# Optimization experiments

Hardware: AMD Instinct MI355X
Metric: run time of the kernel (lower is better)

Reference implementation:

```python
import jax, jax.numpy as jnp
import numpy as np
import math

INPUT_SIZE = 1024
HIDDEN_SIZE = 1024
RANK = 256
BATCH = 32
SEQ = 512


def setup_inputs() -> dict:
    key = jax.random.key(0)
    k_x, k_a, k_b, k_c = jax.random.split(key, 4)
    stdv = 1.0 / math.sqrt(HIDDEN_SIZE)
    x = jax.random.normal(k_x, (BATCH, SEQ, INPUT_SIZE), dtype=jnp.float32)
    a = jax.random.uniform(k_a, (HIDDEN_SIZE, RANK * 4), minval=-stdv, maxval=stdv, dtype=jnp.float32)
    b = jax.random.uniform(k_b, (INPUT_SIZE, RANK * 4), minval=-stdv, maxval=stdv, dtype=jnp.float32)
    ct = jax.random.uniform(k_c, (RANK * 4, HIDDEN_SIZE), minval=-stdv, maxval=stdv, dtype=jnp.float32)
    return {"x": x, "a": a, "b": b, "ct": ct}


def reference(x, a, b, ct):
    B, S, _ = x.shape
    H = a.shape[0]
    R = a.shape[1] // 4
    ct3 = ct.reshape(4, R, H)  # (4, R, H)
    # Precompute input projection for all timesteps: (B, S, 4R)
    xb = jnp.einsum('bsi,ir->bsr', x, b)

    def step(carry, xb_t):
        h, c = carry
        g = (h @ a) * xb_t                      # (B, 4R)
        g = jnp.einsum('bkr,krh->bkh', g.reshape(B, 4, R), ct3)  # (B, 4, H)
        f_t = jax.nn.sigmoid(g[:, 0])
        i_t = jax.nn.sigmoid(g[:, 1])
        g_t = jnp.tanh(g[:, 2])
        o_t = jax.nn.sigmoid(g[:, 3])
        c = f_t * c + i_t * g_t
        h = o_t * jnp.tanh(c)
        return (h, c), h

    h0 = jnp.zeros((B, H), dtype=x.dtype)
    c0 = jnp.zeros((B, H), dtype=x.dtype)
    (h_t, c_t), hs = jax.lax.scan(step, (h0, c0), jnp.swapaxes(xb, 0, 1))
    hidden_seq = jnp.swapaxes(hs, 0, 1)  # (B, S, H)
    return hidden_seq, (h_t, c_t)
```

## Files before the change

kernel.cpp:

```cpp
#include <hip/hip_runtime.h>
#include <math.h>

#define NTHR 512
typedef unsigned long long u64;

__device__ __forceinline__ void st_uc(float* p, float v) {
    asm volatile("global_store_dword %0, %1, off sc0 sc1" :: "v"(p), "v"(v) : "memory");
}
#define LGKM0_BAR do { \
    asm volatile("s_waitcnt lgkmcnt(0)" ::: "memory"); \
    __builtin_amdgcn_s_barrier(); \
} while (0)

__global__ void init_kernel(u64* hp, u64* gp) {
    int i = blockIdx.x * blockDim.x + threadIdx.x;
    if (i < 65536) {
        __hip_atomic_store(hp + i, 0xFFFFFFFF00000000ull, __ATOMIC_RELAXED, __HIP_MEMORY_SCOPE_AGENT);
        __hip_atomic_store(gp + i, 0xFFFFFFFE00000000ull, __ATOMIC_RELAXED, __HIP_MEMORY_SCOPE_AGENT);
    }
}

__global__ __launch_bounds__(256) void xb_gemm(const float* __restrict__ X,
                                               const float* __restrict__ Bw,
                                               float* __restrict__ XB) {
    __shared__ float xs[16][132];
    __shared__ float bs[16][132];
    const int bm = blockIdx.x >> 3;
    const int bn = blockIdx.x & 7;
    const int m0 = bm * 128, n0 = bn * 128;
    const int tid = threadIdx.x;
    const int tx = tid & 15, ty = tid >> 4;
    float acc[8][8];
#pragma unroll
    for (int i = 0; i < 8; ++i)
#pragma unroll
        for (int j = 0; j < 8; ++j) acc[i][j] = 0.f;

    for (int k0 = 0; k0 < 1024; k0 += 16) {
#pragma unroll
        for (int p = 0; p < 2; ++p) {
            int f = tid + p * 256;
            int m = f >> 2, kq = f & 3;
            float4 v = *(const float4*)&X[(size_t)(m0 + m) * 1024 + k0 + kq * 4];
            xs[kq * 4 + 0][m] = v.x; xs[kq * 4 + 1][m] = v.y;
            xs[kq * 4 + 2][m] = v.z; xs[kq * 4 + 3][m] = v.w;
        }
#pragma unroll
        for (int p = 0; p < 2; ++p) {
            int f = tid + p * 256;
            int k = f >> 5, n = (f & 31) * 4;
            float4 v = *(const float4*)&Bw[(size_t)(k0 + k) * 1024 + n0 + n];
            *(float4*)&bs[k][n] = v;
        }
        __syncthreads();
#pragma unroll
        for (int k = 0; k < 16; ++k) {
            float xv[8], bv[8];
            *(float4*)&xv[0] = *(const float4*)&xs[k][ty * 8];
            *(float4*)&xv[4] = *(const float4*)&xs[k][ty * 8 + 4];
            *(float4*)&bv[0] = *(const float4*)&bs[k][tx * 8];
            *(float4*)&bv[4] = *(const float4*)&bs[k][tx * 8 + 4];
#pragma unroll
            for (int i = 0; i < 8; ++i)
#pragma unroll
                for (int j = 0; j < 8; ++j) acc[i][j] += xv[i] * bv[j];
        }
        __syncthreads();
    }
#pragma unroll
    for (int i = 0; i < 8; ++i)
#pragma unroll
        for (int j = 0; j < 8; j += 4) {
            float4 v = make_float4(acc[i][j], acc[i][j + 1], acc[i][j + 2], acc[i][j + 3]);
            *(float4*)&XB[(size_t)(m0 + ty * 8 + i) * 1024 + n0 + tx * 8 + j] = v;
        }
}

__global__ __launch_bounds__(NTHR, 1) void scan_kernel(
    const float* __restrict__ A, const float* __restrict__ CTm,
    float* __restrict__ XBH, u64* __restrict__ hp, u64* __restrict__ gp,
    float* __restrict__ ht_out, float* __restrict__ ct_out) {
    extern __shared__ float lds[];
    float* a_lf  = lds;
    float* ct_lf = lds + 16384;
    float* stgf  = lds + 32768;
    float* scr0  = lds + 36864;
    float* scr1  = lds + 37120;
    const float4* a_l4  = (const float4*)a_lf;
    const float4* ct_l4 = (const float4*)ct_lf;
    float4* stg4 = (float4*)stgf;

    const int wg  = blockIdx.x;
    const int bg0 = wg >> 6;
    const int bg1 = bg0 + 4;
    const int sg  = wg & 63;
    const int c0wg = sg * 16;
    const int tid = threadIdx.x;

    {
        const int c = tid & 15, i0 = tid >> 4;
        for (int i = i0; i < 1024; i += 32) {
            a_lf[c * 1024 + i]  = A[(size_t)i * 1024 + c0wg + c];
            ct_lf[c * 1024 + i] = CTm[(size_t)i * 1024 + c0wg + c];
        }
    }

    const int L  = tid & 63;
    const int w  = tid >> 6;
    const int Lc = L & 7;
    const int Lb = (L >> 3) & 3;
    const int cg = w & 1, kq = w >> 1;

    int wIdx[8], sIdx[4];
#pragma unroll
    for (int c = 0; c < 8; ++c) wIdx[c] = (cg * 8 + (c ^ Lc)) * 256 + kq * 64 + L;
#pragma unroll
    for (int r = 0; r < 4; ++r) sIdx[r] = ((r ^ Lb) << 8) + kq * 64 + L;

    const int e_b   = L >> 4;
    const int e_j   = L & 15;
    const int e_cgo = e_j >> 3;
    const int e_sx  = e_b * 8 + (e_j & 7);
    const int col   = c0wg + e_j;

    float creg = 0.f;
    float xbv  = 0.f;
    u64 qpf[8];

    auto issue_pf = [&](const u64* base) {
#pragma unroll
        for (int j = 0; j < 8; ++j)
            qpf[j] = __hip_atomic_load(base + tid + 512 * j, __ATOMIC_RELAXED,
                                       __HIP_MEMORY_SCOPE_AGENT);
    };

    auto compute = [&](const float4* wmat, float* scr) {
        float4 sv[4], wv[8];
#pragma unroll
        for (int r = 0; r < 4; ++r) sv[r] = stg4[sIdx[r]];
#pragma unroll
        for (int c = 0; c < 8; ++c) wv[c] = wmat[wIdx[c]];
        float v[32];
#pragma unroll
        for (int r = 0; r < 4; ++r)
#pragma unroll
            for (int c = 0; c < 8; ++c)
                v[r * 8 + c] = sv[r].x * wv[c].x + sv[r].y * wv[c].y
                             + sv[r].z * wv[c].z + sv[r].w * wv[c].w;
#pragma unroll
        for (int j = 0; j < 16; ++j) v[j] = v[2 * j] + __shfl_xor(v[2 * j + 1], 1);
#pragma unroll
        for (int j = 0; j < 8; ++j)  v[j] = v[2 * j] + __shfl_xor(v[2 * j + 1], 2);
#pragma unroll
        for (int j = 0; j < 4; ++j)  v[j] = v[2 * j] + __shfl_xor(v[2 * j + 1], 4);
#pragma unroll
        for (int j = 0; j < 2; ++j)  v[j] = v[2 * j] + __shfl_xor(v[2 * j + 1], 8);
        v[0] = v[0] + __shfl_xor(v[1], 16);
        v[0] = v[0] + __shfl_xor(v[0], 32);
        if (L < 32) scr[kq * 64 + cg * 32 + L] = v[0];
    };

    auto epiA_fn = [&](int t, const float* s, int bgx) {
        float q = s[e_cgo * 32 + e_sx] + s[64 + e_cgo * 32 + e_sx]
                + s[128 + e_cgo * 32 + e_sx] + s[192 + e_cgo * 32 + e_sx];
        u64 pk = ((u64)(unsigned)t << 32) | (u64)__float_as_uint(q * xbv);
        __hip_atomic_store(gp + (size_t)(t & 1) * 32768 + (size_t)(bgx * 4 + e_b) * 1024 + col,
                           pk, __ATOMIC_RELAXED, __HIP_MEMORY_SCOPE_AGENT);
    };
    auto epiB_fn = [&](int t, const float* s, int bgx) {
        float q0 = s[e_cgo * 32 + e_sx],       q1 = s[64 + e_cgo * 32 + e_sx];
        float q2 = s[128 + e_cgo * 32 + e_sx], q3 = s[192 + e_cgo * 32 + e_sx];
        float ft = 1.f / (1.f + __expf(-q0));
        float it = 1.f / (1.f + __expf(-q1));
        float gt = tanhf(q2);
        float ot = 1.f / (1.f + __expf(-q3));
        creg = ft * creg + it * gt;
        float hv = ot * tanhf(creg);
        int bglob = bgx * 4 + e_b;
        u64 pk = ((u64)(unsigned)t << 32) | (u64)__float_as_uint(hv);
        __hip_atomic_store(hp + (size_t)(t & 1) * 32768 + (size_t)bglob * 1024 + col,
                           pk, __ATOMIC_RELAXED, __HIP_MEMORY_SCOPE_AGENT);
        st_uc(XBH + ((size_t)bglob * 512 + t) * 1024 + col, hv);
        if (t == 511) {
            st_uc(ht_out + (size_t)bglob * 1024 + col, hv);
            st_uc(ct_out + (size_t)bglob * 1024 + col, creg);
        }
    };

    auto sub = [&](const u64* base, unsigned expect, const float4* wmat, float* scr,
                   int ek, int t, const u64* pfbase) {
        if (ek == 1) { if (w == 4 && t > 0) epiB_fn(t - 1, scr1, bg1); }
        else if (ek == 2) { if (w == 1) epiA_fn(t, scr0, bg0); }
        else if (ek == 3) { if (w == 2) epiA_fn(t, scr1, bg1); }
        else { if (w == 0) epiB_fn(t, scr0, bg0); }
        u64 q[8];
#pragma unroll
        for (int j = 0; j < 8; ++j) q[j] = qpf[j];
        for (;;) {
            bool ok = true;
#pragma unroll
            for (int j = 0; j < 8; ++j) ok &= ((unsigned)(q[j] >> 32) == expect);
            if (!__any(!ok)) break;
            __builtin_amdgcn_s_sleep(1);
#pragma unroll
            for (int j = 0; j < 8; ++j)
                q[j] = __hip_atomic_load(base + tid + 512 * j, __ATOMIC_RELAXED,
                                         __HIP_MEMORY_SCOPE_AGENT);
        }
#pragma unroll
        for (int j = 0; j < 8; ++j) stgf[tid + 512 * j] = __uint_as_float((unsigned)q[j]);
        LGKM0_BAR;
        compute(wmat, scr);
        issue_pf(pfbase);
        LGKM0_BAR;
    };

    __syncthreads();
    issue_pf(hp + 32768 + (size_t)bg0 * 4096);

    for (int k = 0; k < 512; ++k) {
        const unsigned expA = (unsigned)(k - 1);
        const unsigned expB = (unsigned)k;
        if (w == 1) xbv = __uint_as_float(__hip_atomic_load(
            (const unsigned*)(XBH + ((size_t)(bg0 * 4 + e_b) * 512 + k) * 1024 + col),
            __ATOMIC_RELAXED, __HIP_MEMORY_SCOPE_AGENT));
        if (w == 2) xbv = __uint_as_float(__hip_atomic_load(
            (const unsigned*)(XBH + ((size_t)(bg1 * 4 + e_b) * 512 + k) * 1024 + col),
            __ATOMIC_RELAXED, __HIP_MEMORY_SCOPE_AGENT));

        const size_t hsl = (size_t)((k + 1) & 1) * 32768;
        const size_t gsl = (size_t)(k & 1) * 32768;
        sub(hp + hsl + (size_t)bg0 * 4096, expA, a_l4, scr0, 1, k,
            hp + hsl + (size_t)bg1 * 4096);
        sub(hp + hsl + (size_t)bg1 * 4096, expA, a_l4, scr1, 2, k,
            gp + gsl + (size_t)bg0 * 4096);
        sub(gp + gsl + (size_t)bg0 * 4096, expB, ct_l4, scr0, 3, k,
            gp + gsl + (size_t)bg1 * 4096);
        sub(gp + gsl + (size_t)bg1 * 4096, expB, ct_l4, scr1, 4, k,
            hp + (size_t)(k & 1) * 32768 + (size_t)bg0 * 4096);
    }
    if (w == 4) epiB_fn(511, scr1, bg1);
}

extern "C" void kernel_launch(void* const* d_in, const int* in_sizes, int n_in,
                              void* d_out, int out_size, void* d_ws, size_t ws_size,
                              hipStream_t stream) {
    const float* X   = (const float*)d_in[0];
    const float* A   = (const float*)d_in[1];
    const float* Bw  = (const float*)d_in[2];
    const float* CTm = (const float*)d_in[3];

    float* out    = (float*)d_out;
    float* XBH    = out;
    float* ht_out = out + (size_t)32 * 512 * 1024;
    float* ct_out = ht_out + 32 * 1024;

    u64* hp = (u64*)d_ws;
    u64* gp = hp + 65536;

    (void)hipFuncSetAttribute((const void*)scan_kernel,
                              hipFuncAttributeMaxDynamicSharedMemorySize, 149504);

    init_kernel<<<dim3(256), dim3(256), 0, stream>>>(hp, gp);
    xb_gemm<<<dim3(1024), dim3(256), 0, stream>>>(X, Bw, XBH);
    scan_kernel<<<dim3(256), dim3(NTHR), 149504, stream>>>(A, CTm, XBH, hp, gp,
                                                           ht_out, ct_out);
}
```

Before: 4.364 ms.

## Restructure scan step: per-wave column ownership, swizzled LDS, epilogue fused into compute

After: 7.258 ms. 1.66x slower.

```diff
diff --git a/kernel.cpp b/kernel.cpp
--- a/kernel.cpp
+++ b/kernel.cpp
@@ -11,6 +11,15 @@
     asm volatile("s_waitcnt lgkmcnt(0)" ::: "memory"); \
     __builtin_amdgcn_s_barrier(); \
 } while (0)
+
+__device__ __forceinline__ float comp4(float4 v, int b) {
+    float xy = (b & 1) ? v.y : v.x;
+    float zw = (b & 1) ? v.w : v.z;
+    return (b & 2) ? zw : xy;
+}
+#define RED4(a, d) do { \
+    a.x += __shfl_xor(a.x, d); a.y += __shfl_xor(a.y, d); \
+    a.z += __shfl_xor(a.z, d); a.w += __shfl_xor(a.w, d); } while (0)
 
 __global__ void init_kernel(u64* hp, u64* gp) {
     int i = blockIdx.x * blockDim.x + threadIdx.x;
@@ -83,12 +92,10 @@
     extern __shared__ float lds[];
     float* a_lf  = lds;
     float* ct_lf = lds + 16384;
-    float* stgf  = lds + 32768;
-    float* scr0  = lds + 36864;
-    float* scr1  = lds + 37120;
+    float* stg0f = lds + 32768;
+    float* stg1f = lds + 36864;
     const float4* a_l4  = (const float4*)a_lf;
     const float4* ct_l4 = (const float4*)ct_lf;
-    float4* stg4 = (float4*)stgf;
 
     const int wg  = blockIdx.x;
     const int bg0 = wg >> 6;
@@ -100,31 +107,26 @@
     {
         const int c = tid & 15, i0 = tid >> 4;
         for (int i = i0; i < 1024; i += 32) {
-            a_lf[c * 1024 + i]  = A[(size_t)i * 1024 + c0wg + c];
-            ct_lf[c * 1024 + i] = CTm[(size_t)i * 1024 + c0wg + c];
+            int fi = (c << 10) + ((((i >> 2) ^ ((i >> 6) & 7))) << 2) + (i & 3);
+            a_lf[fi]  = A[(size_t)i * 1024 + c0wg + c];
+            ct_lf[fi] = CTm[(size_t)i * 1024 + c0wg + c];
         }
     }
 
     const int L  = tid & 63;
     const int w  = tid >> 6;
-    const int Lc = L & 7;
-    const int Lb = (L >> 3) & 3;
-    const int cg = w & 1, kq = w >> 1;
-
-    int wIdx[8], sIdx[4];
-#pragma unroll
-    for (int c = 0; c < 8; ++c) wIdx[c] = (cg * 8 + (c ^ Lc)) * 256 + kq * 64 + L;
-#pragma unroll
-    for (int r = 0; r < 4; ++r) sIdx[r] = ((r ^ Lb) << 8) + kq * 64 + L;
-
-    const int e_b   = L >> 4;
-    const int e_j   = L & 15;
-    const int e_cgo = e_j >> 3;
-    const int e_sx  = e_b * 8 + (e_j & 7);
-    const int col   = c0wg + e_j;
-
-    float creg = 0.f;
-    float xbv  = 0.f;
+    const int ks = L & 7;
+    const int kw = (L >> 2) & 7;
+    const int gt = L >> 4;
+    const int kb = ((gt << 2) + ((L & 15) >> 2)) & 7;
+    const int lc0 = 2 * w, lc1 = 2 * w + 1;
+    const bool pub = (L < 8);
+    const int p_b = L & 3;
+    const int p_c = (L >> 2) & 1;
+    const int p_col = c0wg + 2 * w + p_c;
+
+    float creg0 = 0.f, creg1 = 0.f;
+    float xb0 = 0.f, xb1 = 0.f;
     u64 qpf[8];
 
     auto issue_pf = [&](const u64* base) {
@@ -134,65 +136,7 @@
                                        __HIP_MEMORY_SCOPE_AGENT);
     };
 
-    auto compute = [&](const float4* wmat, float* scr) {
-        float4 sv[4], wv[8];
-#pragma unroll
-        for (int r = 0; r < 4; ++r) sv[r] = stg4[sIdx[r]];
-#pragma unroll
-        for (int c = 0; c < 8; ++c) wv[c] = wmat[wIdx[c]];
-        float v[32];
-#pragma unroll
-        for (int r = 0; r < 4; ++r)
-#pragma unroll
-            for (int c = 0; c < 8; ++c)
-                v[r * 8 + c] = sv[r].x * wv[c].x + sv[r].y * wv[c].y
-                             + sv[r].z * wv[c].z + sv[r].w * wv[c].w;
-#pragma unroll
-        for (int j = 0; j < 16; ++j) v[j] = v[2 * j] + __shfl_xor(v[2 * j + 1], 1);
-#pragma unroll
-        for (int j = 0; j < 8; ++j)  v[j] = v[2 * j] + __shfl_xor(v[2 * j + 1], 2);
-#pragma unroll
-        for (int j = 0; j < 4; ++j)  v[j] = v[2 * j] + __shfl_xor(v[2 * j + 1], 4);
-#pragma unroll
-        for (int j = 0; j < 2; ++j)  v[j] = v[2 * j] + __shfl_xor(v[2 * j + 1], 8);
-        v[0] = v[0] + __shfl_xor(v[1], 16);
-        v[0] = v[0] + __shfl_xor(v[0], 32);
-        if (L < 32) scr[kq * 64 + cg * 32 + L] = v[0];
-    };
-
-    auto epiA_fn = [&](int t, const float* s, int bgx) {
-        float q = s[e_cgo * 32 + e_sx] + s[64 + e_cgo * 32 + e_sx]
-                + s[128 + e_cgo * 32 + e_sx] + s[192 + e_cgo * 32 + e_sx];
-        u64 pk = ((u64)(unsigned)t << 32) | (u64)__float_as_uint(q * xbv);
-        __hip_atomic_store(gp + (size_t)(t & 1) * 32768 + (size_t)(bgx * 4 + e_b) * 1024 + col,
-                           pk, __ATOMIC_RELAXED, __HIP_MEMORY_SCOPE_AGENT);
-    };
-    auto epiB_fn = [&](int t, const float* s, int bgx) {
-        float q0 = s[e_cgo * 32 + e_sx],       q1 = s[64 + e_cgo * 32 + e_sx];
-        float q2 = s[128 + e_cgo * 32 + e_sx], q3 = s[192 + e_cgo * 32 + e_sx];
-        float ft = 1.f / (1.f + __expf(-q0));
-        float it = 1.f / (1.f + __expf(-q1));
-        float gt = tanhf(q2);
-        float ot = 1.f / (1.f + __expf(-q3));
-        creg = ft * creg + it * gt;
-        float hv = ot * tanhf(creg);
-        int bglob = bgx * 4 + e_b;
-        u64 pk = ((u64)(unsigned)t << 32) | (u64)__float_as_uint(hv);
-        __hip_atomic_store(hp + (size_t)(t & 1) * 32768 + (size_t)bglob * 1024 + col,
-                           pk, __ATOMIC_RELAXED, __HIP_MEMORY_SCOPE_AGENT);
-        st_uc(XBH + ((size_t)bglob * 512 + t) * 1024 + col, hv);
-        if (t == 511) {
-            st_uc(ht_out + (size_t)bglob * 1024 + col, hv);
-            st_uc(ct_out + (size_t)bglob * 1024 + col, creg);
-        }
-    };
-
-    auto sub = [&](const u64* base, unsigned expect, const float4* wmat, float* scr,
-                   int ek, int t, const u64* pfbase) {
-        if (ek == 1) { if (w == 4 && t > 0) epiB_fn(t - 1, scr1, bg1); }
-        else if (ek == 2) { if (w == 1) epiA_fn(t, scr0, bg0); }
-        else if (ek == 3) { if (w == 2) epiA_fn(t, scr1, bg1); }
-        else { if (w == 0) epiB_fn(t, scr0, bg0); }
+    auto stage = [&](const u64* base, unsigned expect, float* stgbuf) {
         u64 q[8];
 #pragma unroll
         for (int j = 0; j < 8; ++j) q[j] = qpf[j];
@@ -208,11 +152,117 @@
                                          __HIP_MEMORY_SCOPE_AGENT);
         }
 #pragma unroll
-        for (int j = 0; j < 8; ++j) stgf[tid + 512 * j] = __uint_as_float((unsigned)q[j]);
+        for (int j = 0; j < 8; ++j) {
+            int p = tid + 512 * j;
+            int k = p & 1023, b = p >> 10;
+            int s = k ^ ((k >> 4) & 7);
+            stgbuf[(s << 2) + b] = __uint_as_float((unsigned)q[j]);
+        }
+    };
+
+    auto computeA = [&](const float* stgbuf, float4& r0, float4& r1) {
+        const float4* hb = (const float4*)stgbuf + (L << 4);
+        const float4* wa = a_l4 + lc0 * 256;
+        const float4* wb = a_l4 + lc1 * 256;
+        float4 a0 = make_float4(0.f, 0.f, 0.f, 0.f), a1 = a0;
+#pragma unroll
+        for (int ii = 0; ii < 4; ++ii) {
+            float4 w0 = wa[((L << 2) + ii) ^ kw];
+            float4 w1 = wb[((L << 2) + ii) ^ kw];
+            float4 h0 = hb[(ii * 4 + 0) ^ ks];
+            float4 h1 = hb[(ii * 4 + 1) ^ ks];
+            float4 h2 = hb[(ii * 4 + 2) ^ ks];
+            float4 h3 = hb[(ii * 4 + 3) ^ ks];
+            a0.x += h0.x*w0.x + h1.x*w0.y + h2.x*w0.z + h3.x*w0.w;
+            a0.y += h0.y*w0.x + h1.y*w0.y + h2.y*w0.z + h3.y*w0.w;
+            a0.z += h0.z*w0.x + h1.z*w0.y + h2.z*w0.z + h3.z*w0.w;
+            a0.w += h0.w*w0.x + h1.w*w0.y + h2.w*w0.z + h3.w*w0.w;
+            a1.x += h0.x*w1.x + h1.x*w1.y + h2.x*w1.z + h3.x*w1.w;
+            a1.y += h0.y*w1.x + h1.y*w1.y + h2.y*w1.z + h3.y*w1.w;
+            a1.z += h0.z*w1.x + h1.z*w1.y + h2.z*w1.z + h3.z*w1.w;
+            a1.w += h0.w*w1.x + h1.w*w1.y + h2.w*w1.z + h3.w*w1.w;
+        }
+        RED4(a0, 1); RED4(a1, 1); RED4(a0, 2); RED4(a1, 2);
+        RED4(a0, 4); RED4(a1, 4); RED4(a0, 8); RED4(a1, 8);
+        RED4(a0, 16); RED4(a1, 16); RED4(a0, 32); RED4(a1, 32);
+        r0 = a0; r1 = a1;
+    };
+    auto computeB = [&](const float* stgbuf, float4& r0, float4& r1) {
+        const float4* gb = (const float4*)stgbuf + (gt << 8) + ((L & 15) << 4);
+        const float4* wa = ct_l4 + lc0 * 256 + (gt << 6);
+        const float4* wb = ct_l4 + lc1 * 256 + (gt << 6);
+        float4 a0 = make_float4(0.f, 0.f, 0.f, 0.f), a1 = a0;
+#pragma unroll
+        for (int ii = 0; ii < 4; ++ii) {
+            int wi = ((L & 15) << 2) + ii;
+            float4 w0 = wa[wi ^ kb];
+            float4 w1 = wb[wi ^ kb];
+            float4 h0 = gb[(ii * 4 + 0) ^ ks];
+            float4 h1 = gb[(ii * 4 + 1) ^ ks];
+            float4 h2 = gb[(ii * 4 + 2) ^ ks];
+            float4 h3 = gb[(ii * 4 + 3) ^ ks];
+            a0.x += h0.x*w0.x + h1.x*w0.y + h2.x*w0.z + h3.x*w0.w;
+            a0.y += h0.y*w0.x + h1.y*w0.y + h2.y*w0.z + h3.y*w0.w;
+            a0.z += h0.z*w0.x + h1.z*w0.y + h2.z*w0.z + h3.z*w0.w;
+            a0.w += h0.w*w0.x + h1.w*w0.y + h2.w*w0.z + h3.w*w0.w;
+            a1.x += h0.x*w1.x + h1.x*w1.y + h2.x*w1.z + h3.x*w1.w;
+            a1.y += h0.y*w1.x + h1.y*w1.y + h2.y*w1.z + h3.y*w1.w;
+            a1.z += h0.z*w1.x + h1.z*w1.y + h2.z*w1.z + h3.z*w1.w;
+            a1.w += h0.w*w1.x + h1.w*w1.y + h2.w*w1.z + h3.w*w1.w;
+        }
+        RED4(a0, 1); RED4(a1, 1); RED4(a0, 2); RED4(a1, 2);
+        RED4(a0, 4); RED4(a1, 4); RED4(a0, 8); RED4(a1, 8);
+        r0 = a0; r1 = a1;
+    };
+
+    auto subA = [&](u64* base, unsigned expect, float* stgbuf, int bgx, float xbv,
+                    u64* pubbase, int t, const u64* pfbase) {
+        stage(base, expect, stgbuf);
         LGKM0_BAR;
-        compute(wmat, scr);
+        float4 r0, r1;
+        computeA(stgbuf, r0, r1);
+        if (pub) {
+            float4 accP = p_c ? r1 : r0;
+            float d = comp4(accP, p_b);
+            u64 pk = ((u64)(unsigned)t << 32) | (u64)__float_as_uint(d * xbv);
+            __hip_atomic_store(pubbase + (size_t)(bgx * 4 + p_b) * 1024 + p_col,
+                               pk, __ATOMIC_RELAXED, __HIP_MEMORY_SCOPE_AGENT);
+        }
         issue_pf(pfbase);
+    };
+    auto subB = [&](u64* base, unsigned expect, float* stgbuf, int bgx, float& creg,
+                    u64* pubbase, int t, const u64* pfbase) {
+        stage(base, expect, stgbuf);
         LGKM0_BAR;
+        float4 r0, r1;
+        computeB(stgbuf, r0, r1);
+        float s0 = comp4(r0, L & 3);
+        float s1 = comp4(r1, L & 3);
+        int src = L & 15;
+        float i0v = __shfl(s0, src + 16), g0v = __shfl(s0, src + 32), o0v = __shfl(s0, src + 48);
+        float i1v = __shfl(s1, src + 16), g1v = __shfl(s1, src + 32), o1v = __shfl(s1, src + 48);
+        if (pub) {
+            float q0 = p_c ? s1 : s0;
+            float q1 = p_c ? i1v : i0v;
+            float q2 = p_c ? g1v : g0v;
+            float q3 = p_c ? o1v : o0v;
+            float ft = 1.f / (1.f + __expf(-q0));
+            float it = 1.f / (1.f + __expf(-q1));
+            float gg = tanhf(q2);
+            float ot = 1.f / (1.f + __expf(-q3));
+            creg = ft * creg + it * gg;
+            float hv = ot * tanhf(creg);
+            int bglob = bgx * 4 + p_b;
+            u64 pk = ((u64)(unsigned)t << 32) | (u64)__float_as_uint(hv);
+            __hip_atomic_store(pubbase + (size_t)bglob * 1024 + p_col,
+                               pk, __ATOMIC_RELAXED, __HIP_MEMORY_SCOPE_AGENT);
+            st_uc(XBH + ((size_t)bglob * 512 + t) * 1024 + p_col, hv);
+            if (t == 511) {
+                st_uc(ht_out + (size_t)bglob * 1024 + p_col, hv);
+                st_uc(ct_out + (size_t)bglob * 1024 + p_col, creg);
+            }
+        }
+        issue_pf(pfbase);
     };
 
     __syncthreads();
@@ -221,25 +271,21 @@
     for (int k = 0; k < 512; ++k) {
         const unsigned expA = (unsigned)(k - 1);
         const unsigned expB = (unsigned)k;
-        if (w == 1) xbv = __uint_as_float(__hip_atomic_load(
-            (const unsigned*)(XBH + ((size_t)(bg0 * 4 + e_b) * 512 + k) * 1024 + col),
-            __ATOMIC_RELAXED, __HIP_MEMORY_SCOPE_AGENT));
-        if (w == 2) xbv = __uint_as_float(__hip_atomic_load(
-            (const unsigned*)(XBH + ((size_t)(bg1 * 4 + e_b) * 512 + k) * 1024 + col),
-            __ATOMIC_RELAXED, __HIP_MEMORY_SCOPE_AGENT));
-
+        if (pub) {
+            xb0 = XBH[((size_t)(bg0 * 4 + p_b) * 512 + k) * 1024 + p_col];
+            xb1 = XBH[((size_t)(bg1 * 4 + p_b) * 512 + k) * 1024 + p_col];
+        }
         const size_t hsl = (size_t)((k + 1) & 1) * 32768;
         const size_t gsl = (size_t)(k & 1) * 32768;
-        sub(hp + hsl + (size_t)bg0 * 4096, expA, a_l4, scr0, 1, k,
-            hp + hsl + (size_t)bg1 * 4096);
-        sub(hp + hsl + (size_t)bg1 * 4096, expA, a_l4, scr1, 2, k,
-            gp + gsl + (size_t)bg0 * 4096);
-        sub(gp + gsl + (size_t)bg0 * 4096, expB, ct_l4, scr0, 3, k,
-            gp + gsl + (size_t)bg1 * 4096);
-        sub(gp + gsl + (size_t)bg1 * 4096, expB, ct_l4, scr1, 4, k,
-            hp + (size_t)(k & 1) * 32768 + (size_t)bg0 * 4096);
+        subA(hp + hsl + (size_t)bg0 * 4096, expA, stg0f, bg0, xb0,
+             gp + gsl, k, hp + hsl + (size_t)bg1 * 4096);
+        subA(hp + hsl + (size_t)bg1 * 4096, expA, stg1f, bg1, xb1,
+             gp + gsl, k, gp + gsl + (size_t)bg0 * 4096);
+        subB(gp + gsl + (size_t)bg0 * 4096, expB, stg0f, bg0, creg0,
+             hp + (size_t)(k & 1) * 32768, k, gp + gsl + (size_t)bg1 * 4096);
+        subB(gp + gsl + (size_t)bg1 * 4096, expB, stg1f, bg1, creg1,
+             hp + (size_t)(k & 1) * 32768, k, hp + (size_t)(k & 1) * 32768 + (size_t)bg0 * 4096);
     }
-    if (w == 4) epiB_fn(511, scr1, bg1);
 }
 
 extern "C" void kernel_launch(void* const* d_in, const int* in_sizes, int n_in,
@@ -259,10 +305,10 @@
     u64* gp = hp + 65536;
 
     (void)hipFuncSetAttribute((const void*)scan_kernel,
-                              hipFuncAttributeMaxDynamicSharedMemorySize, 149504);
+                              hipFuncAttributeMaxDynamicSharedMemorySize, 163840);
 
     init_kernel<<<dim3(256), dim3(256), 0, stream>>>(hp, gp);
     xb_gemm<<<dim3(1024), dim3(256), 0, stream>>>(X, Bw, XBH);
-    scan_kernel<<<dim3(256), dim3(NTHR), 149504, stream>>>(A, CTm, XBH, hp, gp,
+    scan_kernel<<<dim3(256), dim3(NTHR), 163840, stream>>>(A, CTm, XBH, hp, gp,
                                                            ht_out, ct_out);
 }
```
